# Kernel tuning notes

Hardware: AMD Instinct MI355X
Metric: run time of the kernel (lower is better)

Reference implementation:

```python
import jax, jax.numpy as jnp
import numpy as np

N = 4096      # mesh nodes (seq len)
D = 512       # input_dim_nodes / hidden_size
F = 512       # ffn_hidden_size (hidden_dim)
NH = 4        # num_attention_heads
HD = D // NH  # head dim = 128
L = 2         # processor_layers
EPS = 1e-5
SCALE = 1.0 / float(np.sqrt(HD))
NEG = -1e9


def setup_inputs() -> dict:
    key = jax.random.key(0)
    ks = jax.random.split(key, 16)
    nfeat = jax.random.normal(ks[0], (N, D), jnp.float32)
    # sparse graph adjacency mask: True = masked out (TE 'arbitrary' convention)
    mask = jax.random.uniform(ks[1], (N, N)) < 0.99
    idx = jnp.arange(N)
    mask = mask.at[idx, idx].set(False)  # keep self-edges unmasked
    s = 0.02
    p = lambda k, shape: jax.random.normal(k, shape, jnp.float32) * s
    return dict(
        nfeat=nfeat, mask=mask,
        ln1_g=jnp.ones((L, D), jnp.float32), ln1_b=jnp.zeros((L, D), jnp.float32),
        wq=p(ks[2], (L, D, D)), bq=p(ks[3], (L, D)),
        wk=p(ks[4], (L, D, D)), bk=p(ks[5], (L, D)),
        wv=p(ks[6], (L, D, D)), bv=p(ks[7], (L, D)),
        wo=p(ks[8], (L, D, D)), bo=p(ks[9], (L, D)),
        ln2_g=jnp.ones((L, D), jnp.float32), ln2_b=jnp.zeros((L, D), jnp.float32),
        fc1_w=p(ks[10], (L, F, D)), fc1_b=p(ks[11], (L, F)),
        fc2_w=p(ks[12], (L, D, F)), fc2_b=p(ks[13], (L, D)),
    )


def _ln(x, g, b):
    mu = x.mean(-1, keepdims=True)
    var = ((x - mu) ** 2).mean(-1, keepdims=True)
    return (x - mu) * jax.lax.rsqrt(var + EPS) * g + b


def reference(nfeat, mask, ln1_g, ln1_b, wq, bq, wk, bk, wv, bv, wo, bo,
              ln2_g, ln2_b, fc1_w, fc1_b, fc2_w, fc2_b):
    def layer(x, p):
        g1, b1, Wq, Bq, Wk, Bk, Wv, Bv, Wo, Bo, g2, b2, W1, B1, W2, B2 = p
        # --- pre-LN self-attention with arbitrary mask ---
        h = _ln(x, g1, b1)                                  # [N, D]
        q = (h @ Wq.T + Bq).reshape(N, NH, HD)
        k = (h @ Wk.T + Bk).reshape(N, NH, HD)
        v = (h @ Wv.T + Bv).reshape(N, NH, HD)
        scores = jnp.einsum('qhd,khd->hqk', q, k) * SCALE   # [NH, N, N]
        scores = jnp.where(mask[None], NEG, scores)
        attn = jax.nn.softmax(scores, axis=-1)
        o = jnp.einsum('hqk,khd->qhd', attn, v).reshape(N, D)
        x = x + o @ Wo.T + Bo
        # --- pre-LN MLP ---
        h2 = _ln(x, g2, b2)
        m = jax.nn.gelu(h2 @ W1.T + B1, approximate=False) @ W2.T + B2
        return x + m, None

    xs = (ln1_g, ln1_b, wq, bq, wk, bk, wv, bv, wo, bo,
          ln2_g, ln2_b, fc1_w, fc1_b, fc2_w, fc2_b)
    out, _ = jax.lax.scan(layer, nfeat, xs)
    return out
```

## Files before the change

### kernel.cpp

```cpp
#include <hip/hip_runtime.h>
#include <math.h>

#define NN 4096
#define DD 512
#define FF 512
#define CAP 256
#define SCALE 0.08838834764831845f

typedef unsigned short u16;
typedef __attribute__((ext_vector_type(8))) short short8;
typedef __attribute__((ext_vector_type(8))) unsigned short ushort8;
typedef __attribute__((ext_vector_type(4))) unsigned short ushort4v;
typedef __attribute__((ext_vector_type(4))) float floatx4;

__device__ __forceinline__ float bf2f(u16 u) {
    union { unsigned int i; float f; } x; x.i = ((unsigned int)u) << 16; return x.f;
}
__device__ __forceinline__ u16 f2bf(float f) {
    union { float f; unsigned int i; } x; x.f = f;
    unsigned int r = (x.i + 0x7FFFu + ((x.i >> 16) & 1u)) >> 16;
    return (u16)r;
}
__device__ __forceinline__ void gld_lds16(const void* g, void* l) {
    __builtin_amdgcn_global_load_lds((const __attribute__((address_space(1))) void*)g,
                                     (__attribute__((address_space(3))) void*)l, 16, 0, 0);
}

__global__ void build_idx_kernel(const int* __restrict__ mask,
                                 int* __restrict__ idx, int* __restrict__ cnt) {
    int row = blockIdx.x;
    __shared__ int c;
    if (threadIdx.x == 0) c = 0;
    __syncthreads();
    const int4* mrow = (const int4*)(mask + (size_t)row * NN);
    for (int j4 = threadIdx.x; j4 < NN / 4; j4 += blockDim.x) {
        int4 m4 = mrow[j4];
        int base = j4 * 4;
        if (m4.x == 0) idx[row * CAP + atomicAdd(&c, 1)] = base;
        if (m4.y == 0) idx[row * CAP + atomicAdd(&c, 1)] = base + 1;
        if (m4.z == 0) idx[row * CAP + atomicAdd(&c, 1)] = base + 2;
        if (m4.w == 0) idx[row * CAP + atomicAdd(&c, 1)] = base + 3;
    }
    __syncthreads();
    if (threadIdx.x == 0) cnt[row] = (c < CAP) ? c : CAP;
}

struct W6 {
    const float* w[6];
    const float* bq; const float* bk; const float* bv;
};
__global__ void cast_weights(W6 wp, u16* __restrict__ dst, float* __restrict__ bcat) {
    int region = blockIdx.x >> 4;
    int layer = region / 6, mat = region - layer * 6;
    const float* src = wp.w[mat] + (size_t)layer * (DD * DD);
    u16* d = dst + (size_t)region * (DD * DD);
    int off = (blockIdx.x & 15) * 16384 + threadIdx.x * 4;
#pragma unroll
    for (int i = 0; i < 16; i++) {
        int e = off + i * 1024;
        float4 f = *(const float4*)&src[e];
        ushort4v u;
        u.x = f2bf(f.x); u.y = f2bf(f.y); u.z = f2bf(f.z); u.w = f2bf(f.w);
        *(ushort4v*)&d[e] = u;
    }
    if (blockIdx.x < 2) {
        int l = blockIdx.x;
        for (int it = 0; it < 6; it++) {
            int j = it * 256 + threadIdx.x;
            int m = j >> 9, col = j & 511;
            const float* bp = (m == 0) ? wp.bq : (m == 1) ? wp.bk : wp.bv;
            bcat[l * 1536 + j] = bp[l * DD + col];
        }
    }
}

__global__ void ln_kernel(const float* __restrict__ x, const float* __restrict__ g,
                          const float* __restrict__ b, u16* __restrict__ out) {
    int wave = threadIdx.x >> 6, lane = threadIdx.x & 63;
    int row = blockIdx.x * 4 + wave;
    const float* xr = x + (size_t)row * DD;
    float4 p0 = *(const float4*)&xr[lane * 8];
    float4 p1 = *(const float4*)&xr[lane * 8 + 4];
    float v[8] = {p0.x, p0.y, p0.z, p0.w, p1.x, p1.y, p1.z, p1.w};
    float s = 0.f;
#pragma unroll
    for (int i = 0; i < 8; i++) s += v[i];
#pragma unroll
    for (int off = 32; off; off >>= 1) s += __shfl_xor(s, off);
    float mu = s * (1.0f / DD);
    float vs = 0.f;
#pragma unroll
    for (int i = 0; i < 8; i++) { float d = v[i] - mu; vs += d * d; }
#pragma unroll
    for (int off = 32; off; off >>= 1) vs += __shfl_xor(vs, off);
    float r = rsqrtf(vs * (1.0f / DD) + 1e-5f);
    float4 g0 = *(const float4*)&g[lane * 8];
    float4 g1 = *(const float4*)&g[lane * 8 + 4];
    float4 b0 = *(const float4*)&b[lane * 8];
    float4 b1 = *(const float4*)&b[lane * 8 + 4];
    float ge[8] = {g0.x, g0.y, g0.z, g0.w, g1.x, g1.y, g1.z, g1.w};
    float be[8] = {b0.x, b0.y, b0.z, b0.w, b1.x, b1.y, b1.z, b1.w};
    ushort8 ov;
#pragma unroll
    for (int i = 0; i < 8; i++) ov[i] = f2bf((v[i] - mu) * r * ge[i] + be[i]);
    *(ushort8*)&out[(size_t)row * DD + lane * 8] = ov;
}


template <int MODE>
__launch_bounds__(256)
__global__ void gemm_bf16(const u16* __restrict__ A, const u16* __restrict__ B,
                          const float* __restrict__ bias, const float* __restrict__ resIn,
                          float* __restrict__ resOut, u16* __restrict__ outB,
                          int M, int Nout, int K) {
    __shared__ u16 As[64 * 64];
    __shared__ u16 Bs[64 * 64];
    const int m0 = blockIdx.y * 64, n0 = blockIdx.x * 64;
    const int t = threadIdx.x;
    const int wave = t >> 6, lane = t & 63;
    const int wm = (wave & 1) * 32, wn = (wave >> 1) * 32;
    const int sr = t >> 3;
    const int sc = ((((t & 7) - (t >> 3)) & 7)) * 8;
    const int fr = lane & 15, g0 = lane >> 4;

    floatx4 acc[2][2] = {};
    const u16* ag0 = A + (size_t)(m0 + sr) * K + sc;
    const u16* ag1 = A + (size_t)(m0 + 32 + sr) * K + sc;
    const u16* bg0 = B + (size_t)(n0 + sr) * K + sc;
    const u16* bg1 = B + (size_t)(n0 + 32 + sr) * K + sc;
    u16* as0 = As + t * 8;
    u16* as1 = As + 32 * 64 + t * 8;
    u16* bs0 = Bs + t * 8;
    u16* bs1 = Bs + 32 * 64 + t * 8;

    for (int k0 = 0; k0 < K; k0 += 64) {
        __syncthreads();
        gld_lds16(ag0 + k0, as0);
        gld_lds16(ag1 + k0, as1);
        gld_lds16(bg0 + k0, bs0);
        gld_lds16(bg1 + k0, bs1);
        __syncthreads();
#pragma unroll
        for (int h = 0; h < 2; h++) {
            const int fo = (((h << 2) + g0 + fr) & 7) << 3;
            short8 af[2], bf[2];
#pragma unroll
            for (int i = 0; i < 2; i++) af[i] = *(const short8*)&As[(wm + 16 * i + fr) * 64 + fo];
#pragma unroll
            for (int j = 0; j < 2; j++) bf[j] = *(const short8*)&Bs[(wn + 16 * j + fr) * 64 + fo];
#pragma unroll
            for (int i = 0; i < 2; i++)
#pragma unroll
                for (int j = 0; j < 2; j++)
                    acc[i][j] = __builtin_amdgcn_mfma_f32_16x16x32_bf16(af[i], bf[j], acc[i][j], 0, 0, 0);
        }
    }

    const int er = (lane >> 4) * 4, ec = lane & 15;
#pragma unroll
    for (int i = 0; i < 2; i++) {
#pragma unroll
        for (int j = 0; j < 2; j++) {
            int col = n0 + wn + 16 * j + ec;
            float bsv = bias[col];
#pragma unroll
            for (int r = 0; r < 4; r++) {
                int row = m0 + wm + 16 * i + er + r;
                float val = acc[i][j][r] + bsv;
                if (MODE == 1) val = 0.5f * val * (1.0f + erff(val * 0.70710678118654752f));
                if (MODE == 2) {
                    resOut[(size_t)row * Nout + col] = resIn[(size_t)row * Nout + col] + val;
                } else {
                    outB[(size_t)row * Nout + col] = f2bf(val);
                }
            }
        }
    }
}

__launch_bounds__(256)
__global__ void gemm_qkv(const u16* __restrict__ A, const u16* __restrict__ B,
                         const float* __restrict__ bias, u16* __restrict__ outB) {
    __shared__ u16 As[128 * 64];
    __shared__ u16 Bs[64 * 64];
    const int m0 = blockIdx.y * 128, n0 = blockIdx.x * 64;
    const int t = threadIdx.x;
    const int wave = t >> 6, lane = t & 63;
    const int wm = (wave & 1) * 64, wn = (wave >> 1) * 32;
    const int sr = t >> 3;
    const int sc = ((((t & 7) - (t >> 3)) & 7)) * 8;
    const int fr = lane & 15, g0 = lane >> 4;

    floatx4 acc[4][2] = {};
    const u16* agp[4];
    u16* asp[4];
#pragma unroll
    for (int u = 0; u < 4; u++) {
        agp[u] = A + (size_t)(m0 + 32 * u + sr) * DD + sc;
        asp[u] = As + u * (32 * 64) + t * 8;
    }
    const u16* bg0 = B + (size_t)(n0 + sr) * DD + sc;
    const u16* bg1 = B + (size_t)(n0 + 32 + sr) * DD + sc;
    u16* bs0 = Bs + t * 8;
    u16* bs1 = Bs + 32 * 64 + t * 8;

    for (int k0 = 0; k0 < DD; k0 += 64) {
        __syncthreads();
#pragma unroll
        for (int u = 0; u < 4; u++) gld_lds16(agp[u] + k0, asp[u]);
        gld_lds16(bg0 + k0, bs0);
        gld_lds16(bg1 + k0, bs1);
        __syncthreads();
#pragma unroll
        for (int h = 0; h < 2; h++) {
            const int fo = (((h << 2) + g0 + fr) & 7) << 3;
            short8 af[4], bf[2];
#pragma unroll
            for (int i = 0; i < 4; i++) af[i] = *(const short8*)&As[(wm + 16 * i + fr) * 64 + fo];
#pragma unroll
            for (int j = 0; j < 2; j++) bf[j] = *(const short8*)&Bs[(wn + 16 * j + fr) * 64 + fo];
#pragma unroll
            for (int i = 0; i < 4; i++)
#pragma unroll
                for (int j = 0; j < 2; j++)
                    acc[i][j] = __builtin_amdgcn_mfma_f32_16x16x32_bf16(af[i], bf[j], acc[i][j], 0, 0, 0);
        }
    }

    const int er = (lane >> 4) * 4, ec = lane & 15;
#pragma unroll
    for (int j = 0; j < 2; j++) {
        int col = n0 + wn + 16 * j + ec;
        float bsv = bias[col];
#pragma unroll
        for (int i = 0; i < 4; i++) {
#pragma unroll
            for (int r = 0; r < 4; r++) {
                int row = m0 + wm + 16 * i + er + r;
                outB[(size_t)row * 1536 + col] = f2bf(acc[i][j][r] + bsv);
            }
        }
    }
}

__global__ void sparse_attn(const u16* __restrict__ qkv, const int* __restrict__ idx,
                            const int* __restrict__ cnt, u16* __restrict__ o) {
    int t = threadIdx.x;
    int wave = t >> 6, lane = t & 63;
    int qslot = wave >> 1, half = wave & 1;
    int qi = blockIdx.x * 4 + qslot;
    __shared__ float obuf[4][64][8];
    __shared__ float sbuf[4][64];
    __shared__ int sidx[4][CAP];

    int c = cnt[qi];
    const int* ir = idx + qi * CAP;
    for (int j = t & 127; j < c; j += 128) sidx[qslot][j] = ir[j];

    ushort8 qv = *(const ushort8*)(qkv + (size_t)qi * 1536 + lane * 8);
    float qf[8];
#pragma unroll
    for (int e = 0; e < 8; e++) qf[e] = bf2f(qv[e]);
    __syncthreads();

    float sum = 0.f, oa[8] = {};
    int j = half;
    ushort8 kv, vv;
    if (j < c) {
        const u16* kb = qkv + (size_t)sidx[qslot][j] * 1536;
        kv = *(const ushort8*)(kb + 512 + lane * 8);
        vv = *(const ushort8*)(kb + 1024 + lane * 8);
    }
    while (j < c) {
        int jn = j + 2;
        ushort8 kvn, vvn;
        {
            int kjn = (jn < c) ? sidx[qslot][jn] : 0;
            const u16* nb = qkv + (size_t)kjn * 1536;
            kvn = *(const ushort8*)(nb + 512 + lane * 8);
            vvn = *(const ushort8*)(nb + 1024 + lane * 8);
        }
        float d = 0.f;
#pragma unroll
        for (int e = 0; e < 8; e++) d += qf[e] * bf2f(kv[e]);
        d += __shfl_xor(d, 1);
        d += __shfl_xor(d, 2);
        d += __shfl_xor(d, 4);
        d += __shfl_xor(d, 8);
        float p = __expf(d * SCALE);
        sum += p;
#pragma unroll
        for (int e = 0; e < 8; e++) oa[e] += p * bf2f(vv[e]);
        kv = kvn; vv = vvn;
        j = jn;
    }

    if (half == 1) {
#pragma unroll
        for (int e = 0; e < 8; e++) obuf[qslot][lane][e] = oa[e];
        sbuf[qslot][lane] = sum;
    }
    __syncthreads();
    if (half == 0) {
        sum += sbuf[qslot][lane];
        float inv = 1.0f / sum;
        ushort8 ov;
#pragma unroll
        for (int e = 0; e < 8; e++) ov[e] = f2bf((oa[e] + obuf[qslot][lane][e]) * inv);
        *(ushort8*)(o + (size_t)qi * 512 + lane * 8) = ov;
    }
}

extern "C" void kernel_launch(void* const* d_in, const int* in_sizes, int n_in,
                              void* d_out, int out_size, void* d_ws, size_t ws_size,
                              hipStream_t stream) {
    const float* nfeat = (const float*)d_in[0];
    const int*   mask  = (const int*)d_in[1];
    const float* ln1_g = (const float*)d_in[2];
    const float* ln1_b = (const float*)d_in[3];
    const float* bo    = (const float*)d_in[11];
    const float* ln2_g = (const float*)d_in[12];
    const float* ln2_b = (const float*)d_in[13];
    const float* fc1_b = (const float*)d_in[15];
    const float* fc2_b = (const float*)d_in[17];

    const size_t ND = (size_t)NN * DD;
    float* x    = (float*)d_ws;
    u16*   h    = (u16*)(x + ND);
    u16*   qkv  = h + ND;
    u16*   o    = qkv + (size_t)NN * 1536;
    u16*   m1   = o + ND;
    u16*   wc   = m1 + ND;
    float* bcat = (float*)(wc + (size_t)12 * DD * DD);
    int*   idx  = (int*)(bcat + 2 * 1536);
    int*   cnt  = idx + (size_t)NN * CAP;

    W6 w6;
    w6.w[0] = (const float*)d_in[4];  w6.w[1] = (const float*)d_in[6];
    w6.w[2] = (const float*)d_in[8];  w6.w[3] = (const float*)d_in[10];
    w6.w[4] = (const float*)d_in[14]; w6.w[5] = (const float*)d_in[16];
    w6.bq = (const float*)d_in[5]; w6.bk = (const float*)d_in[7]; w6.bv = (const float*)d_in[9];
    cast_weights<<<192, 256, 0, stream>>>(w6, wc, bcat);
    build_idx_kernel<<<NN, 256, 0, stream>>>(mask, idx, cnt);

    const size_t SS = (size_t)DD * DD;
    for (int l = 0; l < 2; l++) {
        size_t bOff = (size_t)l * DD;
        u16* wl = wc + (size_t)l * 6 * SS;
        const float* xin = (l == 0) ? nfeat : x;
        float* fc2_dst = (l == 1) ? (float*)d_out : x;

        ln_kernel<<<NN / 4, 256, 0, stream>>>(xin, ln1_g + bOff, ln1_b + bOff, h);
        gemm_qkv<<<dim3(24, 32), 256, 0, stream>>>(h, wl, bcat + l * 1536, qkv);
        sparse_attn<<<NN / 4, 512, 0, stream>>>(qkv, idx, cnt, o);
        gemm_bf16<2><<<dim3(8, 64), 256, 0, stream>>>(o, wl + 3 * SS, bo + bOff,
                                                      xin, x, nullptr, NN, DD, DD);
        ln_kernel<<<NN / 4, 256, 0, stream>>>(x, ln2_g + bOff, ln2_b + bOff, h);
        gemm_bf16<1><<<dim3(8, 64), 256, 0, stream>>>(h, wl + 4 * SS, fc1_b + bOff,
                                                      nullptr, nullptr, m1, NN, FF, DD);
        gemm_bf16<2><<<dim3(8, 64), 256, 0, stream>>>(m1, wl + 5 * SS, fc2_b + bOff,
                                                      x, fc2_dst, nullptr, NN, DD, FF);
    }
}
```

Measured before the change: 283.7 us.

## Store K/V as interleaved FP8 and Q as fp16 for sparse attention

```diff
diff --git a/kernel.cpp b/kernel.cpp
--- a/kernel.cpp
+++ b/kernel.cpp
@@ -8,10 +8,13 @@
 #define SCALE 0.08838834764831845f
 
 typedef unsigned short u16;
+typedef unsigned char u8;
 typedef __attribute__((ext_vector_type(8))) short short8;
 typedef __attribute__((ext_vector_type(8))) unsigned short ushort8;
 typedef __attribute__((ext_vector_type(4))) unsigned short ushort4v;
 typedef __attribute__((ext_vector_type(4))) float floatx4;
+typedef __attribute__((ext_vector_type(2))) float f32x2;
+typedef _Float16 half8v __attribute__((ext_vector_type(8)));
 
 __device__ __forceinline__ float bf2f(u16 u) {
     union { unsigned int i; float f; } x; x.i = ((unsigned int)u) << 16; return x.f;
@@ -20,6 +23,22 @@
     union { float f; unsigned int i; } x; x.f = f;
     unsigned int r = (x.i + 0x7FFFu + ((x.i >> 16) & 1u)) >> 16;
     return (u16)r;
+}
+__device__ __forceinline__ u16 f2h(float f) {
+    _Float16 h = (_Float16)f;
+    union { _Float16 h; u16 u; } x; x.h = h; return x.u;
+}
+__device__ __forceinline__ u8 f2fp8(float f) {
+    union { _Float16 h; u16 u; } x;
+    x.h = (_Float16)(f * 0.00390625f);
+    u16 h = x.u;
+    h = h + 0x3F + ((h >> 7) & 1);
+    return (u8)(((h >> 8) & 0x80) | ((h >> 7) & 0x7f));
+}
+__device__ __forceinline__ float fp82f_sw(u8 b) {
+    union { u16 u; _Float16 h; } x;
+    x.u = (u16)(((u16)(b & 0x80) << 8) | ((u16)(b & 0x7f) << 7));
+    return (float)x.h * 256.0f;
 }
 __device__ __forceinline__ void gld_lds16(const void* g, void* l) {
     __builtin_amdgcn_global_load_lds((const __attribute__((address_space(1))) void*)g,
@@ -180,7 +199,8 @@
 
 __launch_bounds__(256)
 __global__ void gemm_qkv(const u16* __restrict__ A, const u16* __restrict__ B,
-                         const float* __restrict__ bias, u16* __restrict__ outB) {
+                         const float* __restrict__ bias, u16* __restrict__ qOut,
+                         u8* __restrict__ kv8) {
     __shared__ u16 As[128 * 64];
     __shared__ u16 Bs[64 * 64];
     const int m0 = blockIdx.y * 128, n0 = blockIdx.x * 64;
@@ -228,6 +248,7 @@
     }
 
     const int er = (lane >> 4) * 4, ec = lane & 15;
+    const int bx = blockIdx.x;
 #pragma unroll
     for (int j = 0; j < 2; j++) {
         int col = n0 + wn + 16 * j + ec;
@@ -237,14 +258,24 @@
 #pragma unroll
             for (int r = 0; r < 4; r++) {
                 int row = m0 + wm + 16 * i + er + r;
-                outB[(size_t)row * 1536 + col] = f2bf(acc[i][j][r] + bsv);
+                float val = acc[i][j][r] + bsv;
+                if (bx < 8) {
+                    qOut[(size_t)row * 512 + col] = f2h(val);
+                } else if (bx < 16) {
+                    int cc = col - 512;
+                    kv8[(size_t)row * 1024 + 16 * (cc >> 3) + (cc & 7)] = f2fp8(val);
+                } else {
+                    int cc = col - 1024;
+                    kv8[(size_t)row * 1024 + 16 * (cc >> 3) + 8 + (cc & 7)] = f2fp8(val);
+                }
             }
         }
     }
 }
 
-__global__ void sparse_attn(const u16* __restrict__ qkv, const int* __restrict__ idx,
-                            const int* __restrict__ cnt, u16* __restrict__ o) {
+__global__ void sparse_attn(const u16* __restrict__ q, const u8* __restrict__ kv8,
+                            const int* __restrict__ idx, const int* __restrict__ cnt,
+                            u16* __restrict__ o) {
     int t = threadIdx.x;
     int wave = t >> 6, lane = t & 63;
     int qslot = wave >> 1, half = wave & 1;
@@ -257,32 +288,49 @@
     const int* ir = idx + qi * CAP;
     for (int j = t & 127; j < c; j += 128) sidx[qslot][j] = ir[j];
 
-    ushort8 qv = *(const ushort8*)(qkv + (size_t)qi * 1536 + lane * 8);
+    half8v qv = *(const half8v*)(q + (size_t)qi * 512 + lane * 8);
     float qf[8];
 #pragma unroll
-    for (int e = 0; e < 8; e++) qf[e] = bf2f(qv[e]);
+    for (int e = 0; e < 8; e++) qf[e] = (float)qv[e];
     __syncthreads();
 
     float sum = 0.f, oa[8] = {};
     int j = half;
-    ushort8 kv, vv;
-    if (j < c) {
-        const u16* kb = qkv + (size_t)sidx[qslot][j] * 1536;
-        kv = *(const ushort8*)(kb + 512 + lane * 8);
-        vv = *(const ushort8*)(kb + 1024 + lane * 8);
-    }
+    int4 kvp;
+    if (j < c) kvp = *(const int4*)(kv8 + (size_t)sidx[qslot][j] * 1024 + lane * 16);
     while (j < c) {
         int jn = j + 2;
-        ushort8 kvn, vvn;
+        int4 kvn;
         {
             int kjn = (jn < c) ? sidx[qslot][jn] : 0;
-            const u16* nb = qkv + (size_t)kjn * 1536;
-            kvn = *(const ushort8*)(nb + 512 + lane * 8);
-            vvn = *(const ushort8*)(nb + 1024 + lane * 8);
-        }
+            kvn = *(const int4*)(kv8 + (size_t)kjn * 1024 + lane * 16);
+        }
+        float kd[8], vd[8];
+#if __has_builtin(__builtin_amdgcn_cvt_pk_f32_fp8)
+        {
+            f32x2 p0 = __builtin_amdgcn_cvt_pk_f32_fp8(kvp.x, false);
+            f32x2 p1 = __builtin_amdgcn_cvt_pk_f32_fp8(kvp.x, true);
+            f32x2 p2 = __builtin_amdgcn_cvt_pk_f32_fp8(kvp.y, false);
+            f32x2 p3 = __builtin_amdgcn_cvt_pk_f32_fp8(kvp.y, true);
+            kd[0] = p0.x; kd[1] = p0.y; kd[2] = p1.x; kd[3] = p1.y;
+            kd[4] = p2.x; kd[5] = p2.y; kd[6] = p3.x; kd[7] = p3.y;
+            f32x2 p4 = __builtin_amdgcn_cvt_pk_f32_fp8(kvp.z, false);
+            f32x2 p5 = __builtin_amdgcn_cvt_pk_f32_fp8(kvp.z, true);
+            f32x2 p6 = __builtin_amdgcn_cvt_pk_f32_fp8(kvp.w, false);
+            f32x2 p7 = __builtin_amdgcn_cvt_pk_f32_fp8(kvp.w, true);
+            vd[0] = p4.x; vd[1] = p4.y; vd[2] = p5.x; vd[3] = p5.y;
+            vd[4] = p6.x; vd[5] = p6.y; vd[6] = p7.x; vd[7] = p7.y;
+        }
+#else
+        {
+            const u8* bp = (const u8*)&kvp;
+#pragma unroll
+            for (int e = 0; e < 8; e++) { kd[e] = fp82f_sw(bp[e]); vd[e] = fp82f_sw(bp[8 + e]); }
+        }
+#endif
         float d = 0.f;
 #pragma unroll
-        for (int e = 0; e < 8; e++) d += qf[e] * bf2f(kv[e]);
+        for (int e = 0; e < 8; e++) d = fmaf(qf[e], kd[e], d);
         d += __shfl_xor(d, 1);
         d += __shfl_xor(d, 2);
         d += __shfl_xor(d, 4);
@@ -290,8 +338,8 @@
         float p = __expf(d * SCALE);
         sum += p;
 #pragma unroll
-        for (int e = 0; e < 8; e++) oa[e] += p * bf2f(vv[e]);
-        kv = kvn; vv = vvn;
+        for (int e = 0; e < 8; e++) oa[e] = fmaf(p, vd[e], oa[e]);
+        kvp = kvn;
         j = jn;
     }
 
@@ -327,8 +375,9 @@
     const size_t ND = (size_t)NN * DD;
     float* x    = (float*)d_ws;
     u16*   h    = (u16*)(x + ND);
-    u16*   qkv  = h + ND;
-    u16*   o    = qkv + (size_t)NN * 1536;
+    u16*   q    = h + ND;
+    u8*    kv8  = (u8*)(q + ND);
+    u16*   o    = (u16*)(kv8 + (size_t)NN * 1024);
     u16*   m1   = o + ND;
     u16*   wc   = m1 + ND;
     float* bcat = (float*)(wc + (size_t)12 * DD * DD);
@@ -351,8 +400,8 @@
         float* fc2_dst = (l == 1) ? (float*)d_out : x;
 
         ln_kernel<<<NN / 4, 256, 0, stream>>>(xin, ln1_g + bOff, ln1_b + bOff, h);
-        gemm_qkv<<<dim3(24, 32), 256, 0, stream>>>(h, wl, bcat + l * 1536, qkv);
-        sparse_attn<<<NN / 4, 512, 0, stream>>>(qkv, idx, cnt, o);
+        gemm_qkv<<<dim3(24, 32), 256, 0, stream>>>(h, wl, bcat + l * 1536, q, kv8);
+        sparse_attn<<<NN / 4, 512, 0, stream>>>(q, kv8, idx, cnt, o);
         gemm_bf16<2><<<dim3(8, 64), 256, 0, stream>>>(o, wl + 3 * SS, bo + bOff,
                                                       xin, x, nullptr, NN, DD, DD);
         ln_kernel<<<NN / 4, 256, 0, stream>>>(x, ln2_g + bOff, ln2_b + bOff, h);
```

After: 273.4 us. -3.6%, faster.
